# Kernel optimization log

Measured on AMD Instinct MI355X. Metric: run time of the kernel, lower is better.

The kernel has to match this reference:

```python
import jax, jax.numpy as jnp
import numpy as np

D_MODEL = 1024
N_HEADS = 16
D_K = D_MODEL // N_HEADS


def setup_inputs() -> dict:
    key = jax.random.key(0)
    ks = jax.random.split(key, 11)
    B, S = 4, 2048
    scale = 1.0 / np.sqrt(D_MODEL)
    inp = {
        "Q": jax.random.normal(ks[0], (B, S, D_MODEL), jnp.float32),
        "K": jax.random.normal(ks[1], (B, S, D_MODEL), jnp.float32),
        "V": jax.random.normal(ks[2], (B, S, D_MODEL), jnp.float32),
        "Wq": jax.random.normal(ks[3], (D_MODEL, D_MODEL), jnp.float32) * scale,
        "bq": jnp.zeros((D_MODEL,), jnp.float32),
        "Wk": jax.random.normal(ks[4], (D_MODEL, D_MODEL), jnp.float32) * scale,
        "bk": jnp.zeros((D_MODEL,), jnp.float32),
        "Wv": jax.random.normal(ks[5], (D_MODEL, D_MODEL), jnp.float32) * scale,
        "bv": jnp.zeros((D_MODEL,), jnp.float32),
        "Wo": jax.random.normal(ks[6], (D_MODEL, D_MODEL), jnp.float32) * scale,
        "bo": jnp.zeros((D_MODEL,), jnp.float32),
    }
    return inp


def _split_heads(x):
    B, S, _ = x.shape
    return x.reshape(B, S, N_HEADS, D_K).transpose(0, 2, 1, 3)  # [B,H,S,Dk]


def reference(Q, K, V, Wq, bq, Wk, bk, Wv, bv, Wo, bo):
    # torch nn.Linear: y = x @ W.T + b
    q = _split_heads(Q @ Wq.T + bq)
    k = _split_heads(K @ Wk.T + bk)
    v = _split_heads(V @ Wv.T + bv)
    scores = jnp.einsum("bhsd,bhtd->bhst", q, k) / jnp.sqrt(jnp.float32(D_K))
    probs = jax.nn.softmax(scores, axis=-1)
    attn = jnp.einsum("bhst,bhtd->bhsd", probs, v)  # [B,H,S,Dk]
    B, H, S, Dk = attn.shape
    combined = attn.transpose(0, 2, 1, 3).reshape(B, S, H * Dk)
    return combined @ Wo.T + bo
```

## Files before the change

### kernel.cpp

```cpp
#include <hip/hip_runtime.h>
#include <hip/hip_bf16.h>

typedef float  f32x4  __attribute__((ext_vector_type(4)));
typedef float  f32x16 __attribute__((ext_vector_type(16)));
typedef float  fvec4  __attribute__((ext_vector_type(4)));
typedef __bf16 bf16x8 __attribute__((ext_vector_type(8)));
typedef unsigned short u16x8 __attribute__((ext_vector_type(8)));
typedef unsigned int   u32x4 __attribute__((ext_vector_type(4)));

#define DEVINL __device__ __forceinline__

constexpr int D_MODEL = 1024;
constexpr int NH      = 16;
constexpr int DK      = 64;
constexpr int SEQ     = 2048;
constexpr int BATCH   = 4;
constexpr int M_TOK   = BATCH * SEQ;

DEVINL unsigned short f32_to_bf16_u(float f) {
    unsigned int u = __builtin_bit_cast(unsigned int, f);
    u = (u + 0x7FFFu + ((u >> 16) & 1u)) >> 16;
    return (unsigned short)u;
}

DEVINL float exp2_fast(float x) { return __builtin_amdgcn_exp2f(x); }

DEVINL unsigned cvt_pk_bf16(float lo, float hi_) {
    unsigned d;
    asm("v_cvt_pk_bf16_f32 %0, %1, %2" : "=v"(d) : "v"(lo), "v"(hi_));
    return d;
}

DEVINL void gload_lds16(const void* g, void* l) {
    __builtin_amdgcn_global_load_lds(
        (const __attribute__((address_space(1))) void*)g,
        (__attribute__((address_space(3))) void*)l, 16, 0, 0);
}

__global__ __launch_bounds__(256) void cvt_bf16(const float* __restrict__ src,
                                                unsigned short* __restrict__ dst,
                                                int n8)
{
    int i = blockIdx.x * 256 + threadIdx.x;
    if (i >= n8) return;
    fvec4 v0 = *reinterpret_cast<const fvec4*>(src + (size_t)i * 8);
    fvec4 v1 = *reinterpret_cast<const fvec4*>(src + (size_t)i * 8 + 4);
    bf16x8 o;
    #pragma unroll
    for (int j = 0; j < 4; ++j) { o[j] = (__bf16)v0[j]; o[j + 4] = (__bf16)v1[j]; }
    *reinterpret_cast<bf16x8*>(dst + (size_t)i * 8) = o;
}

template<bool A_BF16, bool SPLIT_HEADS>
__global__ __launch_bounds__(256) void gemm_nt(const void* __restrict__ Ap,
                                               const unsigned short* __restrict__ Wb,
                                               const float* __restrict__ bias,
                                               void* __restrict__ outp,
                                               float out_scale)
{
    constexpr int K = D_MODEL, N = D_MODEL;
    __shared__ char As_[128 * 64 * 2];
    __shared__ char Bs_[128 * 64 * 2];

    const int tid  = threadIdx.x;
    const int lane = tid & 63;
    const int wave = tid >> 6;
    const int wr = (wave >> 1) * 64;
    const int wc = (wave & 1) * 64;
    const int wg = ((int)blockIdx.x & 7) * 64 + ((int)blockIdx.x >> 3);
    const int n0 = (wg & 7) * 128;
    const int m0 = (wg >> 3) * 128;
    const int l15 = lane & 15, h16 = lane >> 4;

    f32x4 acc[4][4] = {};

    for (int kt = 0; kt < K; kt += 64) {
        __syncthreads();
        #pragma unroll
        for (int i = 0; i < 4; ++i) {
            int chunk = tid + i * 256;
            int r = chunk >> 3, c16 = chunk & 7;
            gload_lds16(Wb + (size_t)(n0 + r) * K + kt + c16 * 8, Bs_ + chunk * 16);
        }
        #pragma unroll
        for (int i = 0; i < 4; ++i) {
            int chunk = tid + i * 256;
            int r = chunk >> 3, c16 = chunk & 7;
            if constexpr (A_BF16) {
                gload_lds16((const unsigned short*)Ap + (size_t)(m0 + r) * K + kt + c16 * 8,
                            As_ + chunk * 16);
            } else {
                const float* src = (const float*)Ap + (size_t)(m0 + r) * K + kt + c16 * 8;
                fvec4 v0 = *reinterpret_cast<const fvec4*>(src);
                fvec4 v1 = *reinterpret_cast<const fvec4*>(src + 4);
                bf16x8 o;
                #pragma unroll
                for (int j = 0; j < 4; ++j) { o[j] = (__bf16)v0[j]; o[j + 4] = (__bf16)v1[j]; }
                int boff = (chunk * 16) ^ ((r & 7) << 4);
                *reinterpret_cast<bf16x8*>(As_ + boff) = o;
            }
        }
        __syncthreads();

        #pragma unroll
        for (int kk = 0; kk < 2; ++kk) {
            bf16x8 af[4], bfr[4];
            #pragma unroll
            for (int mi = 0; mi < 4; ++mi) {
                int r = wr + mi * 16 + l15;
                int boff = r * 128 + kk * 64 + h16 * 16;
                if constexpr (!A_BF16) boff ^= (r & 7) << 4;
                af[mi] = *reinterpret_cast<const bf16x8*>(As_ + boff);
            }
            #pragma unroll
            for (int ni = 0; ni < 4; ++ni) {
                int r = wc + ni * 16 + l15;
                bfr[ni] = *reinterpret_cast<const bf16x8*>(Bs_ + r * 128 + kk * 64 + h16 * 16);
            }
            #pragma unroll
            for (int mi = 0; mi < 4; ++mi)
                #pragma unroll
                for (int ni = 0; ni < 4; ++ni)
                    acc[mi][ni] = __builtin_amdgcn_mfma_f32_16x16x32_bf16(
                        af[mi], bfr[ni], acc[mi][ni], 0, 0, 0);
        }
    }

    const int rl = h16 * 4;
    #pragma unroll
    for (int mi = 0; mi < 4; ++mi) {
        #pragma unroll
        for (int ni = 0; ni < 4; ++ni) {
            int col = n0 + wc + ni * 16 + l15;
            float bv = bias[col];
            #pragma unroll
            for (int r = 0; r < 4; ++r) {
                int row = m0 + wr + mi * 16 + rl + r;
                float v = (acc[mi][ni][r] + bv) * out_scale;
                if constexpr (SPLIT_HEADS) {
                    int bb = row >> 11, s = row & (SEQ - 1);
                    int h = col >> 6, dk = col & (DK - 1);
                    ((unsigned short*)outp)[((((size_t)bb * NH + h) * SEQ) + s) * DK + dk]
                        = f32_to_bf16_u(v);
                } else {
                    ((float*)outp)[(size_t)row * N + col] = v;
                }
            }
        }
    }
}

__global__ __launch_bounds__(512, 4) void attn_kernel(const unsigned short* __restrict__ qb,
                                                      const unsigned short* __restrict__ kb,
                                                      const unsigned short* __restrict__ vb,
                                                      unsigned short* __restrict__ ob)
{
    constexpr float THR = 11.0f;
    __shared__ char lds[32768];

    const int tid  = threadIdx.x;
    const int lane = tid & 63;
    const int tl31 = lane & 31;
    const int hi   = lane >> 5;
    const int wave = tid >> 6;
    const int wg   = ((int)blockIdx.x & 7) * 64 + ((int)blockIdx.x >> 3);
    const int bh   = wg >> 3;
    const int q0   = (wg & 7) * 256;
    const size_t base = (size_t)bh * SEQ * DK;

    const int k_kt = tid >> 8, k_kd = (tid >> 6) & 3, k_hi = (tid >> 5) & 1, k_tl = tid & 31;
    const size_t k_goff = base + (size_t)(k_kt * 32 + k_tl) * DK + k_kd * 16 + k_hi * 8;
    const int v_tg = tid >> 6, v_dh = (tid >> 5) & 1, v_dl = tid & 31;
    const size_t v_goff = base + (size_t)(v_tg * 8) * DK + v_dh * 32 + v_dl;

    bf16x8 qf[4];
    #pragma unroll
    for (int kd = 0; kd < 4; ++kd)
        qf[kd] = *reinterpret_cast<const bf16x8*>(
            qb + base + (size_t)(q0 + wave * 32 + tl31) * DK + kd * 16 + hi * 8);

    f32x16 oaccT[2] = {};
    float m_run = -1e30f, l_run = 0.f;

    {
        u16x8 kreg = *reinterpret_cast<const u16x8*>(kb + k_goff);
        unsigned short vg[8];
        #pragma unroll
        for (int j = 0; j < 8; ++j) vg[j] = vb[v_goff + (size_t)j * DK];
        *reinterpret_cast<u16x8*>(lds + tid * 16) = kreg;
        u16x8 vv;
        #pragma unroll
        for (int j = 0; j < 8; ++j) vv[j] = vg[j];
        *reinterpret_cast<u16x8*>(lds + 8192 + tid * 16) = vv;
    }
    __syncthreads();

    for (int t = 0; t < 32; ++t) {
        const int cur = t & 1;
        const char* Kr = lds + cur * 16384;
        const char* Vr = Kr + 8192;

        u16x8 knext;
        unsigned short vg[8];
        if (t < 31) {
            const int t0n = (t + 1) * 64;
            knext = *reinterpret_cast<const u16x8*>(kb + k_goff + (size_t)t0n * DK);
            #pragma unroll
            for (int j = 0; j < 8; ++j) vg[j] = vb[v_goff + (size_t)(t0n + j) * DK];
        }

        f32x16 sT[2] = {};
        #pragma unroll
        for (int kt = 0; kt < 2; ++kt)
            #pragma unroll
            for (int kd = 0; kd < 4; ++kd) {
                bf16x8 kf = *reinterpret_cast<const bf16x8*>(Kr + kt * 4096 + kd * 1024 + lane * 16);
                sT[kt] = __builtin_amdgcn_mfma_f32_32x32x16_bf16(kf, qf[kd], sT[kt], 0, 0, 0);
            }

        float m = sT[0][0];
        #pragma unroll
        for (int kt = 0; kt < 2; ++kt)
            #pragma unroll
            for (int i = 0; i < 16; ++i) m = fmaxf(m, sT[kt][i]);
        m = fmaxf(m, __shfl_xor(m, 32));
        if (__any(m > m_run + THR)) {
            float mn = fmaxf(m_run, m);
            float al = exp2_fast(m_run - mn);
            m_run = mn;
            l_run *= al;
            oaccT[0] *= al;
            oaccT[1] *= al;
        }
        {
            float rs0 = 0.f, rs1 = 0.f, rs2 = 0.f, rs3 = 0.f;
            #pragma unroll
            for (int kt = 0; kt < 2; ++kt)
                #pragma unroll
                for (int i = 0; i < 16; i += 4) {
                    float p0 = exp2_fast(sT[kt][i + 0] - m_run);
                    float p1 = exp2_fast(sT[kt][i + 1] - m_run);
                    float p2 = exp2_fast(sT[kt][i + 2] - m_run);
                    float p3 = exp2_fast(sT[kt][i + 3] - m_run);
                    sT[kt][i + 0] = p0; sT[kt][i + 1] = p1;
                    sT[kt][i + 2] = p2; sT[kt][i + 3] = p3;
                    rs0 += p0; rs1 += p1; rs2 += p2; rs3 += p3;
                }
            float rs = (rs0 + rs1) + (rs2 + rs3);
            rs += __shfl_xor(rs, 32);
            l_run += rs;
        }

        #pragma unroll
        for (int ks = 0; ks < 4; ++ks) {
            bf16x8 vfA0 = *reinterpret_cast<const bf16x8*>(Vr + ks * 2048 + hi * 1024 + tl31 * 16);
            bf16x8 vfA1 = *reinterpret_cast<const bf16x8*>(Vr + ks * 2048 + hi * 1024 + 512 + tl31 * 16);
            const int kt = ks >> 1, b = (ks & 1) * 8;
            unsigned a0 = cvt_pk_bf16(sT[kt][b + 0], sT[kt][b + 1]);
            unsigned a1 = cvt_pk_bf16(sT[kt][b + 2], sT[kt][b + 3]);
            unsigned a2 = cvt_pk_bf16(sT[kt][b + 4], sT[kt][b + 5]);
            unsigned a3 = cvt_pk_bf16(sT[kt][b + 6], sT[kt][b + 7]);
            unsigned z0 = __shfl_xor(hi ? a0 : a2, 32);
            unsigned z1 = __shfl_xor(hi ? a1 : a3, 32);
            u32x4 w;
            w[0] = hi ? z0 : a0;
            w[1] = hi ? z1 : a1;
            w[2] = hi ? a2 : z0;
            w[3] = hi ? a3 : z1;
            bf16x8 pa = __builtin_bit_cast(bf16x8, w);
            oaccT[0] = __builtin_amdgcn_mfma_f32_32x32x16_bf16(vfA0, pa, oaccT[0], 0, 0, 0);
            oaccT[1] = __builtin_amdgcn_mfma_f32_32x32x16_bf16(vfA1, pa, oaccT[1], 0, 0, 0);
        }

        if (t < 31) {
            char* Kw = lds + (cur ^ 1) * 16384;
            *reinterpret_cast<u16x8*>(Kw + tid * 16) = knext;
            u16x8 vv;
            #pragma unroll
            for (int j = 0; j < 8; ++j) vv[j] = vg[j];
            *reinterpret_cast<u16x8*>(Kw + 8192 + tid * 16) = vv;
        }
        __syncthreads();
    }

    char* myregion = lds + wave * 4096;
    const int bb = bh >> 4, h = bh & 15;
    {
        float rl = 1.0f / l_run;
        #pragma unroll
        for (int dh = 0; dh < 2; ++dh)
            #pragma unroll
            for (int r = 0; r < 16; ++r) {
                int dl = (r & 3) + 8 * (r >> 2) + 4 * hi + 32 * dh;
                int boff = (tl31 * 128 + dl * 2) ^ ((tl31 & 7) << 4);
                *reinterpret_cast<unsigned short*>(myregion + boff) =
                    f32_to_bf16_u(oaccT[dh][r] * rl);
            }
        #pragma unroll
        for (int c = 0; c < 4; ++c) {
            int chunk = lane + c * 64;
            int row = chunk >> 3, c16 = chunk & 7;
            int boff = (row * 128 + c16 * 16) ^ ((row & 7) << 4);
            u16x8 v = *reinterpret_cast<const u16x8*>(myregion + boff);
            size_t tok = (size_t)(bb * SEQ) + q0 + wave * 32 + row;
            *reinterpret_cast<u16x8*>(ob + tok * D_MODEL + h * DK + c16 * 8) = v;
        }
    }
}

extern "C" void kernel_launch(void* const* d_in, const int* in_sizes, int n_in,
                              void* d_out, int out_size, void* d_ws, size_t ws_size,
                              hipStream_t stream)
{
    const float* Q  = (const float*)d_in[0];
    const float* K_ = (const float*)d_in[1];
    const float* V  = (const float*)d_in[2];
    const float* Wq = (const float*)d_in[3];
    const float* bq = (const float*)d_in[4];
    const float* Wk = (const float*)d_in[5];
    const float* bk = (const float*)d_in[6];
    const float* Wv = (const float*)d_in[7];
    const float* bv = (const float*)d_in[8];
    const float* Wo = (const float*)d_in[9];
    const float* bo = (const float*)d_in[10];
    float* out = (float*)d_out;

    const size_t SZ = (size_t)M_TOK * D_MODEL;
    const size_t WZ = (size_t)D_MODEL * D_MODEL;
    unsigned short* qh_ = (unsigned short*)d_ws;
    unsigned short* kh_ = qh_ + SZ;
    unsigned short* vh_ = kh_ + SZ;
    unsigned short* ah_ = vh_ + SZ;
    unsigned short* wqb = ah_ + SZ;
    unsigned short* wkb = wqb + WZ;
    unsigned short* wvb = wkb + WZ;
    unsigned short* wob = wvb + WZ;

    const float qscale = 0.125f * 1.4426950408889634f;

    const int cvtg = (int)(WZ / 8 / 256);
    cvt_bf16<<<cvtg, 256, 0, stream>>>(Wq, wqb, (int)(WZ / 8));
    cvt_bf16<<<cvtg, 256, 0, stream>>>(Wk, wkb, (int)(WZ / 8));
    cvt_bf16<<<cvtg, 256, 0, stream>>>(Wv, wvb, (int)(WZ / 8));
    cvt_bf16<<<cvtg, 256, 0, stream>>>(Wo, wob, (int)(WZ / 8));

    gemm_nt<false, true><<<512, 256, 0, stream>>>(Q,  wqb, bq, qh_, qscale);
    gemm_nt<false, true><<<512, 256, 0, stream>>>(K_, wkb, bk, kh_, 1.0f);
    gemm_nt<false, true><<<512, 256, 0, stream>>>(V,  wvb, bv, vh_, 1.0f);
    attn_kernel<<<512, 512, 0, stream>>>(qh_, kh_, vh_, ah_);
    gemm_nt<true, false><<<512, 256, 0, stream>>>(ah_, wob, bo, out, 1.0f);
}
```

Baseline: 224.4 us.

## Write V projection transposed, pre-convert activations to bf16, swizzle GEMM LDS

The V projection GEMM now writes its output in a [B,H,Dk,S] transposed layout, so the attention kernel can load V tiles with one 16-byte vector load instead of eight strided scalar loads. When the workspace is large enough, Q/K/V activations are converted to bf16 in one batched kernel, and the projection GEMMs then use direct global-to-LDS loads. The four weight conversions are merged into a single launch. The GEMM LDS layout is XOR-swizzled for both operands to reduce bank conflicts. In exchange, the activations take an extra full read and bf16 write, and the workspace must hold three more activation-sized buffers.

```diff
diff --git a/kernel.cpp b/kernel.cpp
--- a/kernel.cpp
+++ b/kernel.cpp
@@ -5,6 +5,7 @@
 typedef float  f32x16 __attribute__((ext_vector_type(16)));
 typedef float  fvec4  __attribute__((ext_vector_type(4)));
 typedef __bf16 bf16x8 __attribute__((ext_vector_type(8)));
+typedef unsigned short u16x4 __attribute__((ext_vector_type(4)));
 typedef unsigned short u16x8 __attribute__((ext_vector_type(8)));
 typedef unsigned int   u32x4 __attribute__((ext_vector_type(4)));
 
@@ -37,21 +38,40 @@
         (__attribute__((address_space(3))) void*)l, 16, 0, 0);
 }
 
-__global__ __launch_bounds__(256) void cvt_bf16(const float* __restrict__ src,
-                                                unsigned short* __restrict__ dst,
-                                                int n8)
-{
-    int i = blockIdx.x * 256 + threadIdx.x;
-    if (i >= n8) return;
-    fvec4 v0 = *reinterpret_cast<const fvec4*>(src + (size_t)i * 8);
-    fvec4 v1 = *reinterpret_cast<const fvec4*>(src + (size_t)i * 8 + 4);
+__global__ __launch_bounds__(256) void cvt4(const float* __restrict__ a,
+                                            const float* __restrict__ b,
+                                            const float* __restrict__ c,
+                                            const float* __restrict__ d,
+                                            unsigned short* __restrict__ dst, int n8)
+{
+    int y = blockIdx.y;
+    const float* s = (y == 0) ? a : (y == 1) ? b : (y == 2) ? c : d;
+    size_t i = blockIdx.x * 256 + threadIdx.x;
+    fvec4 v0 = *reinterpret_cast<const fvec4*>(s + i * 8);
+    fvec4 v1 = *reinterpret_cast<const fvec4*>(s + i * 8 + 4);
     bf16x8 o;
     #pragma unroll
     for (int j = 0; j < 4; ++j) { o[j] = (__bf16)v0[j]; o[j + 4] = (__bf16)v1[j]; }
-    *reinterpret_cast<bf16x8*>(dst + (size_t)i * 8) = o;
-}
-
-template<bool A_BF16, bool SPLIT_HEADS>
+    *reinterpret_cast<bf16x8*>(dst + ((size_t)y * n8 + i) * 8) = o;
+}
+
+__global__ __launch_bounds__(256) void cvt3(const float* __restrict__ a,
+                                            const float* __restrict__ b,
+                                            const float* __restrict__ c,
+                                            unsigned short* __restrict__ dst, int n8)
+{
+    int y = blockIdx.y;
+    const float* s = (y == 0) ? a : (y == 1) ? b : c;
+    size_t i = blockIdx.x * 256 + threadIdx.x;
+    fvec4 v0 = *reinterpret_cast<const fvec4*>(s + i * 8);
+    fvec4 v1 = *reinterpret_cast<const fvec4*>(s + i * 8 + 4);
+    bf16x8 o;
+    #pragma unroll
+    for (int j = 0; j < 4; ++j) { o[j] = (__bf16)v0[j]; o[j + 4] = (__bf16)v1[j]; }
+    *reinterpret_cast<bf16x8*>(dst + ((size_t)y * n8 + i) * 8) = o;
+}
+
+template<bool A_BF16, int OMODE>
 __global__ __launch_bounds__(256) void gemm_nt(const void* __restrict__ Ap,
                                                const unsigned short* __restrict__ Wb,
                                                const float* __restrict__ bias,
@@ -80,14 +100,10 @@
         for (int i = 0; i < 4; ++i) {
             int chunk = tid + i * 256;
             int r = chunk >> 3, c16 = chunk & 7;
-            gload_lds16(Wb + (size_t)(n0 + r) * K + kt + c16 * 8, Bs_ + chunk * 16);
-        }
-        #pragma unroll
-        for (int i = 0; i < 4; ++i) {
-            int chunk = tid + i * 256;
-            int r = chunk >> 3, c16 = chunk & 7;
+            int cs = (c16 ^ (r & 7)) * 8;
+            gload_lds16(Wb + (size_t)(n0 + r) * K + kt + cs, Bs_ + chunk * 16);
             if constexpr (A_BF16) {
-                gload_lds16((const unsigned short*)Ap + (size_t)(m0 + r) * K + kt + c16 * 8,
+                gload_lds16((const unsigned short*)Ap + (size_t)(m0 + r) * K + kt + cs,
                             As_ + chunk * 16);
             } else {
                 const float* src = (const float*)Ap + (size_t)(m0 + r) * K + kt + c16 * 8;
@@ -96,8 +112,7 @@
                 bf16x8 o;
                 #pragma unroll
                 for (int j = 0; j < 4; ++j) { o[j] = (__bf16)v0[j]; o[j + 4] = (__bf16)v1[j]; }
-                int boff = (chunk * 16) ^ ((r & 7) << 4);
-                *reinterpret_cast<bf16x8*>(As_ + boff) = o;
+                *reinterpret_cast<bf16x8*>(As_ + ((chunk * 16) ^ ((r & 7) << 4))) = o;
             }
         }
         __syncthreads();
@@ -108,14 +123,14 @@
             #pragma unroll
             for (int mi = 0; mi < 4; ++mi) {
                 int r = wr + mi * 16 + l15;
-                int boff = r * 128 + kk * 64 + h16 * 16;
-                if constexpr (!A_BF16) boff ^= (r & 7) << 4;
-                af[mi] = *reinterpret_cast<const bf16x8*>(As_ + boff);
+                af[mi] = *reinterpret_cast<const bf16x8*>(
+                    As_ + ((r * 128 + kk * 64 + h16 * 16) ^ ((r & 7) << 4)));
             }
             #pragma unroll
             for (int ni = 0; ni < 4; ++ni) {
                 int r = wc + ni * 16 + l15;
-                bfr[ni] = *reinterpret_cast<const bf16x8*>(Bs_ + r * 128 + kk * 64 + h16 * 16);
+                bfr[ni] = *reinterpret_cast<const bf16x8*>(
+                    Bs_ + ((r * 128 + kk * 64 + h16 * 16) ^ ((r & 7) << 4)));
             }
             #pragma unroll
             for (int mi = 0; mi < 4; ++mi)
@@ -133,17 +148,29 @@
         for (int ni = 0; ni < 4; ++ni) {
             int col = n0 + wc + ni * 16 + l15;
             float bv = bias[col];
-            #pragma unroll
-            for (int r = 0; r < 4; ++r) {
-                int row = m0 + wr + mi * 16 + rl + r;
-                float v = (acc[mi][ni][r] + bv) * out_scale;
-                if constexpr (SPLIT_HEADS) {
-                    int bb = row >> 11, s = row & (SEQ - 1);
-                    int h = col >> 6, dk = col & (DK - 1);
-                    ((unsigned short*)outp)[((((size_t)bb * NH + h) * SEQ) + s) * DK + dk]
-                        = f32_to_bf16_u(v);
-                } else {
-                    ((float*)outp)[(size_t)row * N + col] = v;
+            if constexpr (OMODE == 2) {
+                int row0 = m0 + wr + mi * 16 + rl;
+                int bb = row0 >> 11, s0 = row0 & (SEQ - 1);
+                int h = col >> 6, dk = col & (DK - 1);
+                u16x4 o;
+                #pragma unroll
+                for (int r = 0; r < 4; ++r)
+                    o[r] = f32_to_bf16_u((acc[mi][ni][r] + bv) * out_scale);
+                *reinterpret_cast<u16x4*>((unsigned short*)outp +
+                    (((size_t)bb * NH + h) * DK + dk) * SEQ + s0) = o;
+            } else {
+                #pragma unroll
+                for (int r = 0; r < 4; ++r) {
+                    int row = m0 + wr + mi * 16 + rl + r;
+                    float v = (acc[mi][ni][r] + bv) * out_scale;
+                    if constexpr (OMODE == 1) {
+                        int bb = row >> 11, s = row & (SEQ - 1);
+                        int h = col >> 6, dk = col & (DK - 1);
+                        ((unsigned short*)outp)[((((size_t)bb * NH + h) * SEQ) + s) * DK + dk]
+                            = f32_to_bf16_u(v);
+                    } else {
+                        ((float*)outp)[(size_t)row * N + col] = v;
+                    }
                 }
             }
         }
@@ -152,7 +179,7 @@
 
 __global__ __launch_bounds__(512, 4) void attn_kernel(const unsigned short* __restrict__ qb,
                                                       const unsigned short* __restrict__ kb,
-                                                      const unsigned short* __restrict__ vb,
+                                                      const unsigned short* __restrict__ vt,
                                                       unsigned short* __restrict__ ob)
 {
     constexpr float THR = 11.0f;
@@ -166,12 +193,13 @@
     const int wg   = ((int)blockIdx.x & 7) * 64 + ((int)blockIdx.x >> 3);
     const int bh   = wg >> 3;
     const int q0   = (wg & 7) * 256;
-    const size_t base = (size_t)bh * SEQ * DK;
+    const size_t base  = (size_t)bh * SEQ * DK;
+    const size_t baseT = (size_t)bh * DK * SEQ;
 
     const int k_kt = tid >> 8, k_kd = (tid >> 6) & 3, k_hi = (tid >> 5) & 1, k_tl = tid & 31;
     const size_t k_goff = base + (size_t)(k_kt * 32 + k_tl) * DK + k_kd * 16 + k_hi * 8;
     const int v_tg = tid >> 6, v_dh = (tid >> 5) & 1, v_dl = tid & 31;
-    const size_t v_goff = base + (size_t)(v_tg * 8) * DK + v_dh * 32 + v_dl;
+    const size_t v_goff = baseT + (size_t)(v_dh * 32 + v_dl) * SEQ + v_tg * 8;
 
     bf16x8 qf[4];
     #pragma unroll
@@ -184,14 +212,9 @@
 
     {
         u16x8 kreg = *reinterpret_cast<const u16x8*>(kb + k_goff);
-        unsigned short vg[8];
-        #pragma unroll
-        for (int j = 0; j < 8; ++j) vg[j] = vb[v_goff + (size_t)j * DK];
+        u16x8 vreg = *reinterpret_cast<const u16x8*>(vt + v_goff);
         *reinterpret_cast<u16x8*>(lds + tid * 16) = kreg;
-        u16x8 vv;
-        #pragma unroll
-        for (int j = 0; j < 8; ++j) vv[j] = vg[j];
-        *reinterpret_cast<u16x8*>(lds + 8192 + tid * 16) = vv;
+        *reinterpret_cast<u16x8*>(lds + 8192 + tid * 16) = vreg;
     }
     __syncthreads();
 
@@ -200,13 +223,11 @@
         const char* Kr = lds + cur * 16384;
         const char* Vr = Kr + 8192;
 
-        u16x8 knext;
-        unsigned short vg[8];
+        u16x8 kreg, vreg;
         if (t < 31) {
             const int t0n = (t + 1) * 64;
-            knext = *reinterpret_cast<const u16x8*>(kb + k_goff + (size_t)t0n * DK);
-            #pragma unroll
-            for (int j = 0; j < 8; ++j) vg[j] = vb[v_goff + (size_t)(t0n + j) * DK];
+            kreg = *reinterpret_cast<const u16x8*>(kb + k_goff + (size_t)t0n * DK);
+            vreg = *reinterpret_cast<const u16x8*>(vt + v_goff + t0n);
         }
 
         f32x16 sT[2] = {};
@@ -274,11 +295,8 @@
 
         if (t < 31) {
             char* Kw = lds + (cur ^ 1) * 16384;
-            *reinterpret_cast<u16x8*>(Kw + tid * 16) = knext;
-            u16x8 vv;
-            #pragma unroll
-            for (int j = 0; j < 8; ++j) vv[j] = vg[j];
-            *reinterpret_cast<u16x8*>(Kw + 8192 + tid * 16) = vv;
+            *reinterpret_cast<u16x8*>(Kw + tid * 16) = kreg;
+            *reinterpret_cast<u16x8*>(Kw + 8192 + tid * 16) = vreg;
         }
         __syncthreads();
     }
@@ -335,18 +353,25 @@
     unsigned short* wkb = wqb + WZ;
     unsigned short* wvb = wkb + WZ;
     unsigned short* wob = wvb + WZ;
-
+    unsigned short* qbf = wob + WZ;
+    unsigned short* kbf = qbf + SZ;
+    unsigned short* vbf = kbf + SZ;
+
+    const bool big = ws_size >= (size_t)(4 * SZ + 4 * WZ + 3 * SZ) * 2;
     const float qscale = 0.125f * 1.4426950408889634f;
 
-    const int cvtg = (int)(WZ / 8 / 256);
-    cvt_bf16<<<cvtg, 256, 0, stream>>>(Wq, wqb, (int)(WZ / 8));
-    cvt_bf16<<<cvtg, 256, 0, stream>>>(Wk, wkb, (int)(WZ / 8));
-    cvt_bf16<<<cvtg, 256, 0, stream>>>(Wv, wvb, (int)(WZ / 8));
-    cvt_bf16<<<cvtg, 256, 0, stream>>>(Wo, wob, (int)(WZ / 8));
-
-    gemm_nt<false, true><<<512, 256, 0, stream>>>(Q,  wqb, bq, qh_, qscale);
-    gemm_nt<false, true><<<512, 256, 0, stream>>>(K_, wkb, bk, kh_, 1.0f);
-    gemm_nt<false, true><<<512, 256, 0, stream>>>(V,  wvb, bv, vh_, 1.0f);
+    cvt4<<<dim3((int)(WZ / 8 / 256), 4), 256, 0, stream>>>(Wq, Wk, Wv, Wo, wqb, (int)(WZ / 8));
+
+    if (big) {
+        cvt3<<<dim3((int)(SZ / 8 / 256), 3), 256, 0, stream>>>(Q, K_, V, qbf, (int)(SZ / 8));
+        gemm_nt<true, 1><<<512, 256, 0, stream>>>(qbf, wqb, bq, qh_, qscale);
+        gemm_nt<true, 1><<<512, 256, 0, stream>>>(kbf, wkb, bk, kh_, 1.0f);
+        gemm_nt<true, 2><<<512, 256, 0, stream>>>(vbf, wvb, bv, vh_, 1.0f);
+    } else {
+        gemm_nt<false, 1><<<512, 256, 0, stream>>>(Q,  wqb, bq, qh_, qscale);
+        gemm_nt<false, 1><<<512, 256, 0, stream>>>(K_, wkb, bk, kh_, 1.0f);
+        gemm_nt<false, 2><<<512, 256, 0, stream>>>(V,  wvb, bv, vh_, 1.0f);
+    }
     attn_kernel<<<512, 512, 0, stream>>>(qh_, kh_, vh_, ah_);
-    gemm_nt<true, false><<<512, 256, 0, stream>>>(ah_, wob, bo, out, 1.0f);
-}
+    gemm_nt<true, 0><<<512, 256, 0, stream>>>(ah_, wob, bo, out, 1.0f);
+}
```

Result: faster. 217.8 us (-2.9%).
